# Kernel optimization log

Hardware: AMD Instinct MI355X
Metric: run time of the kernel (lower is better)

The kernel has to match this reference:

```python
import jax, jax.numpy as jnp
import numpy as np

QK_DIM = 64
ATTN_BETA = 1.0 / QK_DIM ** 0.5  # default beta = 1/sqrt(qk_dim)


def setup_inputs() -> dict:
    key = jax.random.key(0)
    k1, k2, k3, k4 = jax.random.split(key, 4)
    B, K, D = 8, 1024, 768
    H, Z = 12, 64
    M = int(D * 4.0)
    g = jax.random.normal(k1, (B, K, D), dtype=jnp.float32)
    wq = jax.random.normal(k2, (H, Z, D), dtype=jnp.float32) * 0.02
    wk = jax.random.normal(k3, (H, Z, D), dtype=jnp.float32) * 0.02
    w_hn = jax.random.normal(k4, (M, D), dtype=jnp.float32) * (1.0 / np.sqrt(D))
    beta_hn = jnp.ones((1,), dtype=jnp.float32) * 0.01
    return {"g": g, "wq": wq, "wk": wk, "w_hn": w_hn, "beta_hn": beta_hn}


def reference(g, wq, wk, w_hn, beta_hn):
    # Attention energy: q,k = per-head projections; E = -1/beta * sum logsumexp(beta * QK^T)
    q = jnp.einsum('bkd,hzd->bkhz', g, wq)  # [B,K,H,Z]
    k = jnp.einsum('bkd,hzd->bkhz', g, wk)  # [B,K,H,Z]
    A = jnp.einsum('bqhz,bkhz->bhqk', q, k)  # [B,H,Q,K]
    attn_e = -1.0 / ATTN_BETA * jnp.sum(jax.nn.logsumexp(ATTN_BETA * A, axis=-1))
    # Hopfield energy: E = -1/beta_hn * sum logsumexp(beta_hn * g W^T)
    h = beta_hn * jnp.einsum('bkd,md->bkm', g, w_hn)  # [B,K,M]
    hn_e = -1.0 / beta_hn * jnp.sum(jax.nn.logsumexp(h, axis=-1))  # shape (1,)
    return attn_e + hn_e  # shape (1,) matching torch broadcast
```

## Files before the change

kernel.cpp:

```cpp
#include <hip/hip_runtime.h>
#include <hip/hip_bf16.h>
#include <stdint.h>
#include <stddef.h>

typedef __bf16 bf16;
typedef __bf16 bf16x4 __attribute__((ext_vector_type(4)));
typedef __bf16 bf16x8 __attribute__((ext_vector_type(8)));
typedef float  f32x4  __attribute__((ext_vector_type(4)));

#define LOG2E 1.44269504f
#define QSCALE 0.18033688f

__device__ __forceinline__ void gld_lds16(const void* gptr, void* lptr) {
    __builtin_amdgcn_global_load_lds(
        (const __attribute__((address_space(1))) unsigned int*)gptr,
        (__attribute__((address_space(3))) unsigned int*)lptr,
        16, 0, 0);
}

__global__ void cast_all(const float* __restrict__ g, const float* __restrict__ wq,
                         const float* __restrict__ wk, const float* __restrict__ whn,
                         bf16* __restrict__ g_bf, bf16* __restrict__ Wcat,
                         float* __restrict__ rowsum, float* __restrict__ out) {
    int b = blockIdx.x, t = threadIdx.x;
    if (b < 8) {
        float4 z = {0.f, 0.f, 0.f, 0.f};
        *(float4*)(rowsum + (b * 256 + t) * 4) = z;
        if (b == 0 && t == 0) out[0] = 0.f;
    }
    const float* src; bf16* dst; int off;
    if (b < 6144)      { src = g;   dst = g_bf;           off = 0;    }
    else if (b < 6720) { src = wq;  dst = Wcat;           off = 6144; }
    else if (b < 7296) { src = wk;  dst = Wcat + 589824;  off = 6720; }
    else               { src = whn; dst = Wcat + 1179648; off = 7296; }
    int i = ((b - off) * 256 + t) * 4;
    float4 v = *(const float4*)(src + i);
    bf16x4 o = { (bf16)v.x, (bf16)v.y, (bf16)v.z, (bf16)v.w };
    *(bf16x4*)(dst + i) = o;
}

__global__ void gemm_fused(const bf16* __restrict__ A, const bf16* __restrict__ Bm,
                           bf16* __restrict__ qkh, float* __restrict__ rowsum,
                           const float* __restrict__ beta_p) {
    __shared__ __align__(16) bf16 As[128 * 64];
    __shared__ __align__(16) bf16 Bs[128 * 64];
    const int t = threadIdx.x;
    const int w = t >> 6, l = t & 63;
    const int wm = (w >> 1) * 64, wn = (w & 1) * 64;
    const int tile_m = blockIdx.x * 128;
    const int tile_n = blockIdx.y * 128;

    f32x4 acc[4][4];
#pragma unroll
    for (int i = 0; i < 4; i++)
#pragma unroll
        for (int j = 0; j < 4; j++)
#pragma unroll
            for (int q = 0; q < 4; q++) acc[i][j][q] = 0.f;

    const int srow = t >> 3;
    const int sswz = (t & 7) ^ (srow & 7);
    const bf16* gA = A  + (size_t)(tile_m + srow) * 768 + sswz * 8;
    const bf16* gB = Bm + (size_t)(tile_n + srow) * 768 + sswz * 8;

    const int fr = l & 15, fg = l >> 4;

    for (int k0 = 0; k0 < 768; k0 += 64) {
#pragma unroll
        for (int i = 0; i < 4; i++) {
            gld_lds16(gA + (size_t)i * 32 * 768 + k0, As + (i * 256 + t) * 8);
            gld_lds16(gB + (size_t)i * 32 * 768 + k0, Bs + (i * 256 + t) * 8);
        }
        __builtin_amdgcn_s_waitcnt(0);
        __syncthreads();

#pragma unroll
        for (int ks = 0; ks < 2; ks++) {
            const int swz = (((ks * 4 + fg) ^ (fr & 7))) * 8;
            bf16x8 af[4], bfr[4];
#pragma unroll
            for (int i = 0; i < 4; i++) {
                af[i]  = *(const bf16x8*)(As + (wm + i * 16 + fr) * 64 + swz);
                bfr[i] = *(const bf16x8*)(Bs + (wn + i * 16 + fr) * 64 + swz);
            }
#pragma unroll
            for (int i = 0; i < 4; i++)
#pragma unroll
                for (int j = 0; j < 4; j++)
                    acc[i][j] = __builtin_amdgcn_mfma_f32_16x16x32_bf16(af[i], bfr[j], acc[i][j], 0, 0, 0);
        }
        __syncthreads();
    }

    const int cr = fg * 4, cc = fr;

    if (tile_n < 1536) {
        const int tt = (tile_n >= 768);
        const int hh = (tile_n - tt * 768 + wn) >> 6;
        const int bb = tile_m >> 10;
        const int m7 = tile_m & 1023;
        const float sc = tt ? 1.0f : QSCALE;
        bf16* base = qkh + ((size_t)(((bb * 12 + hh) * 2 + tt) * 1024 + m7) << 6);
#pragma unroll
        for (int i = 0; i < 4; i++)
#pragma unroll
            for (int r = 0; r < 4; r++) {
                int kr  = wm + i * 16 + cr + r;
                int swz = (cr + r) & 7;
#pragma unroll
                for (int j = 0; j < 4; j++) {
                    int z   = j * 16 + cc;
                    int pos = (((z >> 3) ^ swz) << 3) | (z & 7);
                    base[(size_t)kr * 64 + pos] = (bf16)(sc * acc[i][j][r]);
                }
            }
    } else {
        const float sc2 = beta_p[0] * LOG2E;
#pragma unroll
        for (int i = 0; i < 4; i++)
#pragma unroll
            for (int r = 0; r < 4; r++) {
                float s = 0.f;
#pragma unroll
                for (int j = 0; j < 4; j++) s += __builtin_amdgcn_exp2f(sc2 * acc[i][j][r]);
                s += __shfl_xor(s, 1, 16);
                s += __shfl_xor(s, 2, 16);
                s += __shfl_xor(s, 4, 16);
                s += __shfl_xor(s, 8, 16);
                if ((l & 15) == 0)
                    atomicAdd(&rowsum[tile_m + wm + i * 16 + cr + r], s);
            }
    }
}

__global__ void __launch_bounds__(256, 4)
attn_energy(const bf16* __restrict__ qkh, float* __restrict__ arow) {
    __shared__ __align__(16) bf16 S[2][128 * 64];
    const int t = threadIdx.x, w = t >> 6, l = t & 63;
    const int qt = blockIdx.x, h = blockIdx.y, b = blockIdx.z;
    const bf16* qp = qkh + ((size_t)((b * 12 + h) * 2 + 0) << 16) + qt * 128 * 64;
    const bf16* kp = qkh + ((size_t)((b * 12 + h) * 2 + 1) << 16);
    const int fr = l & 15, fg = l >> 4;

#pragma unroll
    for (int i = 0; i < 4; i++)
        gld_lds16(qp + (i * 256 + t) * 8, S[0] + (i * 256 + t) * 8);
    __builtin_amdgcn_s_waitcnt(0);
    __syncthreads();

    bf16x8 af[2][2];
#pragma unroll
    for (int mi = 0; mi < 2; mi++)
#pragma unroll
        for (int ks = 0; ks < 2; ks++) {
            int r = w * 32 + mi * 16 + fr;
            af[mi][ks] = *(const bf16x8*)(S[0] + r * 64 + ((ks * 4 + fg) ^ (fr & 7)) * 8);
        }

#pragma unroll
    for (int i = 0; i < 4; i++)
        gld_lds16(kp + (i * 256 + t) * 8, S[1] + (i * 256 + t) * 8);

    float rs[2][4] = {};
    for (int kc = 0; kc < 8; kc++) {
        const bf16* Sc = S[1 - (kc & 1)];
        __builtin_amdgcn_s_waitcnt(0);
        __syncthreads();
        if (kc < 7) {
            const bf16* src = kp + (kc + 1) * 128 * 64;
            bf16* dstb = (bf16*)S[kc & 1];
#pragma unroll
            for (int i = 0; i < 4; i++)
                gld_lds16(src + (i * 256 + t) * 8, dstb + (i * 256 + t) * 8);
        }
#pragma unroll
        for (int nt = 0; nt < 8; nt++) {
            int kr = nt * 16 + fr;
            bf16x8 b0 = *(const bf16x8*)(Sc + kr * 64 + ((0 + fg) ^ (fr & 7)) * 8);
            bf16x8 b1 = *(const bf16x8*)(Sc + kr * 64 + ((4 + fg) ^ (fr & 7)) * 8);
#pragma unroll
            for (int mi = 0; mi < 2; mi++) {
                f32x4 acc;
#pragma unroll
                for (int q = 0; q < 4; q++) acc[q] = 0.f;
                acc = __builtin_amdgcn_mfma_f32_16x16x32_bf16(af[mi][0], b0, acc, 0, 0, 0);
                acc = __builtin_amdgcn_mfma_f32_16x16x32_bf16(af[mi][1], b1, acc, 0, 0, 0);
#pragma unroll
                for (int r = 0; r < 4; r++) rs[mi][r] += __builtin_amdgcn_exp2f(acc[r]);
            }
        }
    }

    const int rowbase = (b * 12 + h) * 1024 + qt * 128 + w * 32;
#pragma unroll
    for (int mi = 0; mi < 2; mi++)
#pragma unroll
        for (int r = 0; r < 4; r++) {
            float v = rs[mi][r];
            v += __shfl_xor(v, 1, 16);
            v += __shfl_xor(v, 2, 16);
            v += __shfl_xor(v, 4, 16);
            v += __shfl_xor(v, 8, 16);
            if ((l & 15) == 0)
                arow[rowbase + mi * 16 + fg * 4 + r] = v;
        }
}

__global__ void finalize(const float* __restrict__ sums, const float* __restrict__ beta_p,
                         float* __restrict__ out) {
    __shared__ float wpart[4];
    const int t = threadIdx.x, w = t >> 6, l = t & 63;
    const int i = blockIdx.x * 256 + t;
    float v;
    if (i < 8192) v = (-1.f / beta_p[0]) * __logf(sums[i]);
    else          v = -8.f * __logf(sums[i]);
    for (int o = 32; o > 0; o >>= 1) v += __shfl_down(v, o, 64);
    if (l == 0) wpart[w] = v;
    __syncthreads();
    if (t == 0) atomicAdd(out, wpart[0] + wpart[1] + wpart[2] + wpart[3]);
}

extern "C" void kernel_launch(void* const* d_in, const int* in_sizes, int n_in,
                              void* d_out, int out_size, void* d_ws, size_t ws_size,
                              hipStream_t stream) {
    const float* g    = (const float*)d_in[0];
    const float* wq   = (const float*)d_in[1];
    const float* wk   = (const float*)d_in[2];
    const float* w_hn = (const float*)d_in[3];
    const float* beta = (const float*)d_in[4];
    float* out = (float*)d_out;

    char* ws = (char*)d_ws;
    bf16*  g_bf   = (bf16*)(ws);
    bf16*  Wcat   = (bf16*)(ws + 12582912);
    bf16*  qkh    = (bf16*)(ws + 19660800);
    float* sums   = (float*)(ws + 44826624);
    float* rowsum = sums;
    float* arow   = sums + 8192;

    cast_all<<<9600, 256, 0, stream>>>(g, wq, wk, w_hn, g_bf, Wcat, rowsum, out);

    dim3 gg(64, 36);
    gemm_fused<<<gg, 256, 0, stream>>>(g_bf, Wcat, qkh, rowsum, beta);

    dim3 ga(8, 12, 8);
    attn_energy<<<ga, 256, 0, stream>>>(qkh, arow);

    finalize<<<416, 256, 0, stream>>>(sums, beta, out);
}
```

Before: 177.2 us.

## Quantize projection GEMM inputs to FP8 and use scaled MFMA 16x16x128

Inputs and weights are now cast to FP8 (e4m3) instead of bf16, with the weights pre-scaled by 16 to keep them in range, and the fused projection GEMM runs on the MX-scaled FP8 MFMA with a K-step of 128. Epilogue scales undo the weight scaling. This halves the bytes written by the cast kernel and read by the GEMM, and doubles MFMA throughput per instruction. In exchange the projections and the Hopfield energy lose accuracy, which may break tolerance.

```diff
diff --git a/kernel.cpp b/kernel.cpp
--- a/kernel.cpp
+++ b/kernel.cpp
@@ -7,9 +7,13 @@
 typedef __bf16 bf16x4 __attribute__((ext_vector_type(4)));
 typedef __bf16 bf16x8 __attribute__((ext_vector_type(8)));
 typedef float  f32x4  __attribute__((ext_vector_type(4)));
-
-#define LOG2E 1.44269504f
+typedef int    i32x8  __attribute__((ext_vector_type(8)));
+typedef unsigned char u8;
+
+#define LOG2E  1.44269504f
 #define QSCALE 0.18033688f
+#define WSC    16.0f
+#define IWSC   0.0625f
 
 __device__ __forceinline__ void gld_lds16(const void* gptr, void* lptr) {
     __builtin_amdgcn_global_load_lds(
@@ -20,7 +24,7 @@
 
 __global__ void cast_all(const float* __restrict__ g, const float* __restrict__ wq,
                          const float* __restrict__ wk, const float* __restrict__ whn,
-                         bf16* __restrict__ g_bf, bf16* __restrict__ Wcat,
+                         u8* __restrict__ g_f8, u8* __restrict__ Wcat,
                          float* __restrict__ rowsum, float* __restrict__ out) {
     int b = blockIdx.x, t = threadIdx.x;
     if (b < 8) {
@@ -28,22 +32,23 @@
         *(float4*)(rowsum + (b * 256 + t) * 4) = z;
         if (b == 0 && t == 0) out[0] = 0.f;
     }
-    const float* src; bf16* dst; int off;
-    if (b < 6144)      { src = g;   dst = g_bf;           off = 0;    }
-    else if (b < 6720) { src = wq;  dst = Wcat;           off = 6144; }
-    else if (b < 7296) { src = wk;  dst = Wcat + 589824;  off = 6720; }
-    else               { src = whn; dst = Wcat + 1179648; off = 7296; }
+    const float* src; u8* dst; int off; float sc;
+    if (b < 6144)      { src = g;   dst = g_f8;           off = 0;    sc = 1.0f; }
+    else if (b < 6720) { src = wq;  dst = Wcat;           off = 6144; sc = WSC;  }
+    else if (b < 7296) { src = wk;  dst = Wcat + 589824;  off = 6720; sc = WSC;  }
+    else               { src = whn; dst = Wcat + 1179648; off = 7296; sc = WSC;  }
     int i = ((b - off) * 256 + t) * 4;
     float4 v = *(const float4*)(src + i);
-    bf16x4 o = { (bf16)v.x, (bf16)v.y, (bf16)v.z, (bf16)v.w };
-    *(bf16x4*)(dst + i) = o;
-}
-
-__global__ void gemm_fused(const bf16* __restrict__ A, const bf16* __restrict__ Bm,
+    int p = __builtin_amdgcn_cvt_pk_fp8_f32(sc * v.x, sc * v.y, 0, false);
+    p     = __builtin_amdgcn_cvt_pk_fp8_f32(sc * v.z, sc * v.w, p, true);
+    *(int*)(dst + i) = p;
+}
+
+__global__ void gemm_fused(const u8* __restrict__ A, const u8* __restrict__ Bm,
                            bf16* __restrict__ qkh, float* __restrict__ rowsum,
                            const float* __restrict__ beta_p) {
-    __shared__ __align__(16) bf16 As[128 * 64];
-    __shared__ __align__(16) bf16 Bs[128 * 64];
+    __shared__ __align__(16) u8 As[128 * 128];
+    __shared__ __align__(16) u8 Bs[128 * 128];
     const int t = threadIdx.x;
     const int w = t >> 6, l = t & 63;
     const int wm = (w >> 1) * 64, wn = (w & 1) * 64;
@@ -60,35 +65,44 @@
 
     const int srow = t >> 3;
     const int sswz = (t & 7) ^ (srow & 7);
-    const bf16* gA = A  + (size_t)(tile_m + srow) * 768 + sswz * 8;
-    const bf16* gB = Bm + (size_t)(tile_n + srow) * 768 + sswz * 8;
+    const u8* gA = A  + (size_t)(tile_m + srow) * 768 + sswz * 16;
+    const u8* gB = Bm + (size_t)(tile_n + srow) * 768 + sswz * 16;
 
     const int fr = l & 15, fg = l >> 4;
-
-    for (int k0 = 0; k0 < 768; k0 += 64) {
+    const int s0 = ((2 * fg)     ^ (fr & 7)) * 16;
+    const int s1 = ((2 * fg + 1) ^ (fr & 7)) * 16;
+
+    for (int k0 = 0; k0 < 768; k0 += 128) {
 #pragma unroll
         for (int i = 0; i < 4; i++) {
-            gld_lds16(gA + (size_t)i * 32 * 768 + k0, As + (i * 256 + t) * 8);
-            gld_lds16(gB + (size_t)i * 32 * 768 + k0, Bs + (i * 256 + t) * 8);
+            gld_lds16(gA + (size_t)i * 32 * 768 + k0, As + (i * 256 + t) * 16);
+            gld_lds16(gB + (size_t)i * 32 * 768 + k0, Bs + (i * 256 + t) * 16);
         }
         __builtin_amdgcn_s_waitcnt(0);
         __syncthreads();
 
-#pragma unroll
-        for (int ks = 0; ks < 2; ks++) {
-            const int swz = (((ks * 4 + fg) ^ (fr & 7))) * 8;
-            bf16x8 af[4], bfr[4];
-#pragma unroll
-            for (int i = 0; i < 4; i++) {
-                af[i]  = *(const bf16x8*)(As + (wm + i * 16 + fr) * 64 + swz);
-                bfr[i] = *(const bf16x8*)(Bs + (wn + i * 16 + fr) * 64 + swz);
-            }
-#pragma unroll
-            for (int i = 0; i < 4; i++)
-#pragma unroll
-                for (int j = 0; j < 4; j++)
-                    acc[i][j] = __builtin_amdgcn_mfma_f32_16x16x32_bf16(af[i], bfr[j], acc[i][j], 0, 0, 0);
-        }
+        union F8 { uint4 q[2]; i32x8 v; };
+        i32x8 af[4], bfr[4];
+#pragma unroll
+        for (int i = 0; i < 4; i++) {
+            const u8* ra = As + (wm + i * 16 + fr) * 128;
+            const u8* rb = Bs + (wn + i * 16 + fr) * 128;
+            F8 ua, ub;
+            ua.q[0] = *(const uint4*)(ra + s0);
+            ua.q[1] = *(const uint4*)(ra + s1);
+            ub.q[0] = *(const uint4*)(rb + s0);
+            ub.q[1] = *(const uint4*)(rb + s1);
+            af[i] = ua.v; bfr[i] = ub.v;
+        }
+#pragma unroll
+        for (int i = 0; i < 4; i++)
+#pragma unroll
+            for (int j = 0; j < 4; j++)
+                acc[i][j] = __builtin_amdgcn_mfma_scale_f32_16x16x128_f8f6f4(
+                    af[i], bfr[j], acc[i][j],
+                    0, 0,
+                    0, 0x7F7F7F7F,
+                    0, 0x7F7F7F7F);
         __syncthreads();
     }
 
@@ -99,7 +113,7 @@
         const int hh = (tile_n - tt * 768 + wn) >> 6;
         const int bb = tile_m >> 10;
         const int m7 = tile_m & 1023;
-        const float sc = tt ? 1.0f : QSCALE;
+        const float sc = (tt ? 1.0f : QSCALE) * IWSC;
         bf16* base = qkh + ((size_t)(((bb * 12 + hh) * 2 + tt) * 1024 + m7) << 6);
 #pragma unroll
         for (int i = 0; i < 4; i++)
@@ -115,7 +129,7 @@
                 }
             }
     } else {
-        const float sc2 = beta_p[0] * LOG2E;
+        const float sc2 = beta_p[0] * LOG2E * IWSC;
 #pragma unroll
         for (int i = 0; i < 4; i++)
 #pragma unroll
@@ -231,17 +245,17 @@
     float* out = (float*)d_out;
 
     char* ws = (char*)d_ws;
-    bf16*  g_bf   = (bf16*)(ws);
-    bf16*  Wcat   = (bf16*)(ws + 12582912);
-    bf16*  qkh    = (bf16*)(ws + 19660800);
-    float* sums   = (float*)(ws + 44826624);
+    u8*    g_f8   = (u8*)(ws);
+    u8*    Wcat   = (u8*)(ws + 6291456);
+    bf16*  qkh    = (bf16*)(ws + 9830400);
+    float* sums   = (float*)(ws + 34996224);
     float* rowsum = sums;
     float* arow   = sums + 8192;
 
-    cast_all<<<9600, 256, 0, stream>>>(g, wq, wk, w_hn, g_bf, Wcat, rowsum, out);
+    cast_all<<<9600, 256, 0, stream>>>(g, wq, wk, w_hn, g_f8, Wcat, rowsum, out);
 
     dim3 gg(64, 36);
-    gemm_fused<<<gg, 256, 0, stream>>>(g_bf, Wcat, qkh, rowsum, beta);
+    gemm_fused<<<gg, 256, 0, stream>>>(g_f8, Wcat, qkh, rowsum, beta);
 
     dim3 ga(8, 12, 8);
     attn_energy<<<ga, 256, 0, stream>>>(qkh, arow);
```

After: 151.2 us. 14.7% less time.
